# Kernel tuning notes

Measured on AMD Instinct MI355X. Metric: run time of the kernel, lower is better.

## Reference

```python
import jax, jax.numpy as jnp
import numpy as np

H, I, BS = 4096, 14336, 128   # hidden, intermediate, quant blocksize
B, S = 4, 2048                # batch, seq_len


def _dequant(w_int, s, blocksize):
    # w_int: [in, out] int8-valued weights; s: [in//blocksize, out] per-block scales.
    # Each contiguous block of `blocksize` input rows shares one scale.
    return w_int.astype(jnp.float32) * jnp.repeat(s, blocksize, axis=0)


def setup_inputs() -> dict:
    key = jax.random.key(0)
    k = jax.random.split(key, 7)
    x = jax.random.normal(k[0], (B, S, H), dtype=jnp.float32)
    w0 = jax.random.randint(k[1], (H, I), -127, 128, dtype=jnp.int32)  # gate proj (int8 values)
    w1 = jax.random.randint(k[2], (H, I), -127, 128, dtype=jnp.int32)  # up proj
    w2 = jax.random.randint(k[3], (I, H), -127, 128, dtype=jnp.int32)  # down proj
    # small positive per-block scales, typical magnitude for int8 weight quant
    s0 = jax.random.uniform(k[4], (H // BS, I), dtype=jnp.float32) * 0.02 + 1e-3
    s1 = jax.random.uniform(k[5], (H // BS, I), dtype=jnp.float32) * 0.02 + 1e-3
    s2 = jax.random.uniform(k[6], (I // BS, H), dtype=jnp.float32) * 0.02 + 1e-3
    return {"x": x, "w0": w0, "w1": w1, "w2": w2,
            "s0": s0, "s1": s1, "s2": s2, "blocksize": BS}


def reference(x, w0, w1, w2, s0, s1, s2, blocksize):
    # Fused w8a16 gated MLP: out = (silu(x @ W0) * (x @ W1)) @ W2
    W0 = _dequant(w0, s0, blocksize)  # [H, I]
    W1 = _dequant(w1, s1, blocksize)  # [H, I]
    W2 = _dequant(w2, s2, blocksize)  # [I, H]
    g = jnp.einsum('bsh,hi->bsi', x, W0)   # gate
    u = jnp.einsum('bsh,hi->bsi', x, W1)   # up
    h = jax.nn.silu(g) * u                 # [B, S, I]
    return jnp.einsum('bsi,ih->bsh', h, W2)  # same shape as x
```

## Files before the change

### kernel.cpp

```cpp
#include <hip/hip_runtime.h>
#include <cstdint>

#define H_DIM 4096
#define I_DIM 14336
#define M_TOT 8192
#define NI_DIM (2 * I_DIM)

typedef __bf16 bf16_t;
typedef bf16_t bf16x8_t __attribute__((ext_vector_type(8)));
typedef float f32x4_t __attribute__((ext_vector_type(4)));

#define AS1 __attribute__((address_space(1)))
#define AS3 __attribute__((address_space(3)))

static __device__ __forceinline__ unsigned short f2bf(float f) {
  union { float f; unsigned int u; } v; v.f = f;
  unsigned int r = ((v.u >> 16) & 1u) + 0x7FFFu;
  return (unsigned short)((v.u + r) >> 16);
}

static __device__ __forceinline__ void gl2lds16(const void* g, void* l) {
  __builtin_amdgcn_global_load_lds((AS1 void*)(void*)g, (AS3 void*)l, 16, 0, 0);
}

__global__ void k_cvt_x(const float* __restrict__ x,
                        unsigned short* __restrict__ xb, long n4) {
  long i = (long)blockIdx.x * blockDim.x + threadIdx.x;
  const long stride = (long)gridDim.x * blockDim.x;
  for (; i < n4; i += stride) {
    float4 v = ((const float4*)x)[i];
    ushort4 o;
    o.x = f2bf(v.x); o.y = f2bf(v.y); o.z = f2bf(v.z); o.w = f2bf(v.w);
    ((ushort4*)xb)[i] = o;
  }
}

__global__ void k_dequant_t(const int* __restrict__ w, const float* __restrict__ s,
                            unsigned short* __restrict__ wt, int K, int N,
                            int ioff) {
  __shared__ __align__(16) float tile[64 * 68];
  const int n0 = blockIdx.x * 64;
  const int k0 = blockIdx.y * 64;
  const int t = threadIdx.x;
  const int tx = t & 15;
  const int ty = t >> 4;
#pragma unroll
  for (int i = 0; i < 4; ++i) {
    const long gk = k0 + i * 16 + ty;
    const int4 wv = *(const int4*)(w + gk * N + (n0 + tx * 4));
    const float4 sv = *(const float4*)(s + (gk >> 7) * (long)N + (n0 + tx * 4));
    float4 o;
    o.x = (float)wv.x * sv.x;
    o.y = (float)wv.y * sv.y;
    o.z = (float)wv.z * sv.z;
    o.w = (float)wv.w * sv.w;
    *(float4*)(&tile[(i * 16 + ty) * 68 + tx * 4]) = o;
  }
  __syncthreads();
  const int nl = t >> 2;
  const int kc = (t & 3) << 4;
  unsigned int pk[8];
#pragma unroll
  for (int j = 0; j < 8; ++j) {
    unsigned int lo = f2bf(tile[(kc + 2 * j) * 68 + nl]);
    unsigned int hi = f2bf(tile[(kc + 2 * j + 1) * 68 + nl]);
    pk[j] = lo | (hi << 16);
  }
  const int n = n0 + nl;
  const long orow = (ioff < 0) ? (long)n
                               : (long)(((n >> 4) << 5) + (n & 15) + ioff);
  const long base = orow * K + (k0 + kc);
  uint4* dst = (uint4*)(wt + base);
  dst[0] = make_uint4(pk[0], pk[1], pk[2], pk[3]);
  dst[1] = make_uint4(pk[4], pk[5], pk[6], pk[7]);
}

template <int KDIM, int EPI>
__global__ __launch_bounds__(512, 1) void k_gemm_pipe(
    const unsigned short* __restrict__ A,
    const unsigned short* __restrict__ B,
    void* __restrict__ Cout, int Ntiles) {
  __shared__ __align__(16) unsigned short lds[3 * 24576];
  constexpr int KT = KDIM / 64;

  const int nwg = 32 * Ntiles;
  int id = blockIdx.x;
  id = (id & 7) * (nwg >> 3) + (id >> 3);
  const int per = 16 * Ntiles;
  const int grp = id / per;
  const int wi = id - grp * per;
  const int mt = grp * 16 + (wi & 15);
  const int nt = wi >> 4;
  const long m0 = (long)mt * 256;
  const long n0 = (long)nt * 128;

  const int t = threadIdx.x;
  const int lane = t & 63;
  const int wave = t >> 6;
  const int wm = wave >> 1;
  const int wn = wave & 1;

  const int srow = t >> 3;
  const int scol = (((t & 7) ^ (srow & 7)) << 3);
  const unsigned short* gA[4];
  const unsigned short* gB[2];
#pragma unroll
  for (int r = 0; r < 4; ++r)
    gA[r] = A + (m0 + r * 64 + srow) * (long)KDIM + scol;
#pragma unroll
  for (int r = 0; r < 2; ++r)
    gB[r] = B + (n0 + r * 64 + srow) * (long)KDIM + scol;
  unsigned short* sbase = &lds[wave * 512];

  const int colb = ((lane >> 4) ^ (lane & 7)) << 3;
  int aoff[4], boff[4];
#pragma unroll
  for (int mi = 0; mi < 4; ++mi)
    aoff[mi] = (wm * 64 + mi * 16 + (lane & 15)) * 64 + colb;
#pragma unroll
  for (int ni = 0; ni < 4; ++ni)
    boff[ni] = 16384 + (wn * 64 + ni * 16 + (lane & 15)) * 64 + colb;

  auto stage3A = [&](int kt2, int bs) {
    const long ko = (long)kt2 * 64;
    unsigned short* d = sbase + bs * 24576;
    gl2lds16(gA[0] + ko, d);
    gl2lds16(gA[1] + ko, d + 4096);
    gl2lds16(gA[2] + ko, d + 8192);
  };
  auto stage1A2B = [&](int kt2, int bs) {
    const long ko = (long)kt2 * 64;
    unsigned short* d = sbase + bs * 24576;
    gl2lds16(gA[3] + ko, d + 12288);
    gl2lds16(gB[0] + ko, d + 16384);
    gl2lds16(gB[1] + ko, d + 20480);
  };

  f32x4_t acc[4][4];
  const f32x4_t fz = {0.f, 0.f, 0.f, 0.f};
#pragma unroll
  for (int mi = 0; mi < 4; ++mi)
#pragma unroll
    for (int ni = 0; ni < 4; ++ni) acc[mi][ni] = fz;

  stage3A(0, 0); stage1A2B(0, 0);
  stage3A(1, 1); stage1A2B(1, 1);

  int bi = 0;
  for (int kt = 0; kt < KT; ++kt) {
    if (kt != KT - 1)
      asm volatile("s_waitcnt vmcnt(6)" ::: "memory");
    else
      asm volatile("s_waitcnt vmcnt(0)" ::: "memory");
    __builtin_amdgcn_s_barrier();

    const unsigned short* lb = &lds[bi * 24576];
    const int bs = (bi == 0) ? 2 : bi - 1;
    const bool pre = (kt + 2 < KT);

    bf16x8_t af[4], bfv[4];
#pragma unroll
    for (int mi = 0; mi < 4; ++mi) af[mi] = *(const bf16x8_t*)(lb + aoff[mi]);
#pragma unroll
    for (int ni = 0; ni < 4; ++ni) bfv[ni] = *(const bf16x8_t*)(lb + boff[ni]);
    if (pre) stage3A(kt + 2, bs);
    __builtin_amdgcn_s_barrier();
    asm volatile("s_waitcnt lgkmcnt(0)" ::: "memory");
    __builtin_amdgcn_sched_barrier(0);
    __builtin_amdgcn_s_setprio(1);
#pragma unroll
    for (int mi = 0; mi < 4; ++mi)
#pragma unroll
      for (int ni = 0; ni < 4; ++ni)
        acc[mi][ni] = __builtin_amdgcn_mfma_f32_16x16x32_bf16(
            af[mi], bfv[ni], acc[mi][ni], 0, 0, 0);
    __builtin_amdgcn_s_setprio(0);

#pragma unroll
    for (int mi = 0; mi < 4; ++mi)
      af[mi] = *(const bf16x8_t*)(lb + (aoff[mi] ^ 32));
#pragma unroll
    for (int ni = 0; ni < 4; ++ni)
      bfv[ni] = *(const bf16x8_t*)(lb + (boff[ni] ^ 32));
    if (pre) stage1A2B(kt + 2, bs);
    __builtin_amdgcn_s_barrier();
    asm volatile("s_waitcnt lgkmcnt(0)" ::: "memory");
    __builtin_amdgcn_sched_barrier(0);
    __builtin_amdgcn_s_setprio(1);
#pragma unroll
    for (int mi = 0; mi < 4; ++mi)
#pragma unroll
      for (int ni = 0; ni < 4; ++ni)
        acc[mi][ni] = __builtin_amdgcn_mfma_f32_16x16x32_bf16(
            af[mi], bfv[ni], acc[mi][ni], 0, 0, 0);
    __builtin_amdgcn_s_setprio(0);

    bi = (bi == 2) ? 0 : bi + 1;
  }

  const long mr0 = m0 + wm * 64 + ((lane >> 4) << 2);
  if constexpr (EPI == 1) {
    unsigned short* h = (unsigned short*)Cout;
    const int col0 = (int)(n0 >> 1) + wn * 32 + (lane & 15);
#pragma unroll
    for (int mi = 0; mi < 4; ++mi) {
#pragma unroll
      for (int p = 0; p < 2; ++p) {
        const long c = col0 + p * 16;
#pragma unroll
        for (int r = 0; r < 4; ++r) {
          const float gg = acc[mi][2 * p][r];
          const float uu = acc[mi][2 * p + 1][r];
          const float sg = gg / (1.0f + __expf(-gg));
          h[(mr0 + mi * 16 + r) * (long)I_DIM + c] = f2bf(sg * uu);
        }
      }
    }
  } else {
    float* o = (float*)Cout;
    const int col0 = (int)n0 + wn * 64 + (lane & 15);
#pragma unroll
    for (int mi = 0; mi < 4; ++mi)
#pragma unroll
      for (int ni = 0; ni < 4; ++ni)
#pragma unroll
        for (int r = 0; r < 4; ++r)
          o[(mr0 + mi * 16 + r) * (long)H_DIM + (col0 + ni * 16)] =
              acc[mi][ni][r];
  }
}

extern "C" void kernel_launch(void* const* d_in, const int* in_sizes, int n_in,
                              void* d_out, int out_size, void* d_ws, size_t ws_size,
                              hipStream_t stream) {
  const float* x  = (const float*)d_in[0];
  const int* w0   = (const int*)d_in[1];
  const int* w1   = (const int*)d_in[2];
  const int* w2   = (const int*)d_in[3];
  const float* s0 = (const float*)d_in[4];
  const float* s1 = (const float*)d_in[5];
  const float* s2 = (const float*)d_in[6];
  float* out = (float*)d_out;

  char* p = (char*)d_ws;
  unsigned short* xb   = (unsigned short*)p;
  unsigned short* w01t = (unsigned short*)(p + (long)M_TOT * H_DIM * 2);
  unsigned short* hb   = (unsigned short*)(p + (long)M_TOT * H_DIM * 2 +
                                           (long)NI_DIM * H_DIM * 2);
  unsigned short* w2t  = (unsigned short*)p;

  k_cvt_x<<<8192, 256, 0, stream>>>(x, xb, (long)M_TOT * H_DIM / 4);

  k_dequant_t<<<dim3(I_DIM / 64, H_DIM / 64), 256, 0, stream>>>(
      w0, s0, w01t, H_DIM, I_DIM, 0);
  k_dequant_t<<<dim3(I_DIM / 64, H_DIM / 64), 256, 0, stream>>>(
      w1, s1, w01t, H_DIM, I_DIM, 16);

  k_gemm_pipe<H_DIM, 1><<<(M_TOT / 256) * (NI_DIM / 128), 512, 0, stream>>>(
      xb, w01t, hb, NI_DIM / 128);

  k_dequant_t<<<dim3(H_DIM / 64, I_DIM / 64), 256, 0, stream>>>(
      w2, s2, w2t, I_DIM, H_DIM, -1);

  k_gemm_pipe<I_DIM, 2><<<(M_TOT / 256) * (H_DIM / 128), 512, 0, stream>>>(
      hb, w2t, out, H_DIM / 128);
}
```

Baseline: 3.436 ms.

## Switch GEMM to 256x256 tiles with 8-wave quadrant ping-pong pipeline

Replaces the 256x128 GEMM tile with a 256x256 tile where each of 8 waves computes a 128x64 sub-block (8x4 MFMA accumulators). The schedule becomes double-buffered LDS with four compute phases per k-step, each interleaving partial A/B reloads with global-to-LDS staging of the next tiles. The aim is to raise arithmetic intensity and cut global and LDS traffic per FLOP. The cost is more accumulator registers and 128KB of LDS, so effectively one workgroup per CU despite launch_bounds(512,2), plus more barriers per iteration.

```diff
diff --git a/kernel.cpp b/kernel.cpp
--- a/kernel.cpp
+++ b/kernel.cpp
@@ -76,11 +76,11 @@
 }
 
 template <int KDIM, int EPI>
-__global__ __launch_bounds__(512, 1) void k_gemm_pipe(
+__global__ __launch_bounds__(512, 2) void k_gemm8(
     const unsigned short* __restrict__ A,
     const unsigned short* __restrict__ B,
     void* __restrict__ Cout, int Ntiles) {
-  __shared__ __align__(16) unsigned short lds[3 * 24576];
+  __shared__ __align__(16) unsigned short lds[65536];
   constexpr int KT = KDIM / 64;
 
   const int nwg = 32 * Ntiles;
@@ -92,78 +92,76 @@
   const int mt = grp * 16 + (wi & 15);
   const int nt = wi >> 4;
   const long m0 = (long)mt * 256;
-  const long n0 = (long)nt * 128;
+  const long n0 = (long)nt * 256;
 
   const int t = threadIdx.x;
   const int lane = t & 63;
   const int wave = t >> 6;
-  const int wm = wave >> 1;
-  const int wn = wave & 1;
-
-  const int srow = t >> 3;
-  const int scol = (((t & 7) ^ (srow & 7)) << 3);
-  const unsigned short* gA[4];
-  const unsigned short* gB[2];
-#pragma unroll
-  for (int r = 0; r < 4; ++r)
-    gA[r] = A + (m0 + r * 64 + srow) * (long)KDIM + scol;
-#pragma unroll
-  for (int r = 0; r < 2; ++r)
-    gB[r] = B + (n0 + r * 64 + srow) * (long)KDIM + scol;
-  unsigned short* sbase = &lds[wave * 512];
-
-  const int colb = ((lane >> 4) ^ (lane & 7)) << 3;
-  int aoff[4], boff[4];
+  const int wm = wave >> 2;
+  const int wn = wave & 3;
+
+  const int srow = lane >> 3;
+  const int scol = ((lane & 7) ^ srow) << 3;
+  const unsigned short* pA = A + (m0 + wave * 16 + srow) * (long)KDIM + scol;
+  const unsigned short* pB = B + (n0 + wave * 16 + srow) * (long)KDIM + scol;
+  const int ldst = wave * 1024;
+
+  const int lr = lane & 15;
+  const int pch = ((lane >> 4) ^ (lane & 7)) << 3;
+  int aof[4], bof[4];
 #pragma unroll
   for (int mi = 0; mi < 4; ++mi)
-    aoff[mi] = (wm * 64 + mi * 16 + (lane & 15)) * 64 + colb;
-#pragma unroll
-  for (int ni = 0; ni < 4; ++ni)
-    boff[ni] = 16384 + (wn * 64 + ni * 16 + (lane & 15)) * 64 + colb;
-
-  auto stage3A = [&](int kt2, int bs) {
-    const long ko = (long)kt2 * 64;
-    unsigned short* d = sbase + bs * 24576;
-    gl2lds16(gA[0] + ko, d);
-    gl2lds16(gA[1] + ko, d + 4096);
-    gl2lds16(gA[2] + ko, d + 8192);
+    aof[mi] = wm * 8192 + (mi * 16 + lr) * 64 + pch;
+#pragma unroll
+  for (int nj = 0; nj < 4; ++nj)
+    bof[nj] = 16384 + (wn >> 1) * 8192 +
+              ((wn & 1) * 64 + nj * 16 + lr) * 64 + pch;
+
+  auto stgA = [&](int tile, int half, int buf) {
+    const long go = (long)half * 128 * KDIM + (long)tile * 64;
+    unsigned short* d = &lds[buf * 32768 + half * 8192 + ldst];
+    gl2lds16(pA + go, d);
+    gl2lds16(pA + go + 8 * (long)KDIM, d + 512);
   };
-  auto stage1A2B = [&](int kt2, int bs) {
-    const long ko = (long)kt2 * 64;
-    unsigned short* d = sbase + bs * 24576;
-    gl2lds16(gA[3] + ko, d + 12288);
-    gl2lds16(gB[0] + ko, d + 16384);
-    gl2lds16(gB[1] + ko, d + 20480);
+  auto stgB = [&](int tile, int half, int buf) {
+    const long go = (long)half * 128 * KDIM + (long)tile * 64;
+    unsigned short* d = &lds[buf * 32768 + 16384 + half * 8192 + ldst];
+    gl2lds16(pB + go, d);
+    gl2lds16(pB + go + 8 * (long)KDIM, d + 512);
   };
 
-  f32x4_t acc[4][4];
+  f32x4_t acc[8][4];
   const f32x4_t fz = {0.f, 0.f, 0.f, 0.f};
 #pragma unroll
-  for (int mi = 0; mi < 4; ++mi)
-#pragma unroll
-    for (int ni = 0; ni < 4; ++ni) acc[mi][ni] = fz;
-
-  stage3A(0, 0); stage1A2B(0, 0);
-  stage3A(1, 1); stage1A2B(1, 1);
-
-  int bi = 0;
+  for (int mi = 0; mi < 8; ++mi)
+#pragma unroll
+    for (int nj = 0; nj < 4; ++nj) acc[mi][nj] = fz;
+
+  stgB(0, 0, 0); stgB(0, 1, 0);
+  stgA(0, 0, 0); stgA(0, 1, 0);
+  stgB(1, 0, 1); stgB(1, 1, 1);
+  asm volatile("s_waitcnt vmcnt(4)" ::: "memory");
+  __builtin_amdgcn_s_barrier();
+
+  bf16x8_t af[4][2], b0[2][2], b1[2][2];
+
   for (int kt = 0; kt < KT; ++kt) {
-    if (kt != KT - 1)
-      asm volatile("s_waitcnt vmcnt(6)" ::: "memory");
-    else
-      asm volatile("s_waitcnt vmcnt(0)" ::: "memory");
-    __builtin_amdgcn_s_barrier();
-
-    const unsigned short* lb = &lds[bi * 24576];
-    const int bs = (bi == 0) ? 2 : bi - 1;
-    const bool pre = (kt + 2 < KT);
-
-    bf16x8_t af[4], bfv[4];
-#pragma unroll
-    for (int mi = 0; mi < 4; ++mi) af[mi] = *(const bf16x8_t*)(lb + aoff[mi]);
-#pragma unroll
-    for (int ni = 0; ni < 4; ++ni) bfv[ni] = *(const bf16x8_t*)(lb + boff[ni]);
-    if (pre) stage3A(kt + 2, bs);
+    const int cb = kt & 1;
+    const unsigned short* lb = &lds[cb * 32768];
+    const bool pa = (kt + 1 < KT);
+    const bool pb = (kt + 2 < KT);
+
+#pragma unroll
+    for (int mi = 0; mi < 4; ++mi) {
+      af[mi][0] = *(const bf16x8_t*)(lb + aof[mi]);
+      af[mi][1] = *(const bf16x8_t*)(lb + (aof[mi] ^ 32));
+    }
+#pragma unroll
+    for (int nj = 0; nj < 2; ++nj) {
+      b0[nj][0] = *(const bf16x8_t*)(lb + bof[nj]);
+      b0[nj][1] = *(const bf16x8_t*)(lb + (bof[nj] ^ 32));
+    }
+    if (pa) stgA(kt + 1, 0, cb ^ 1);
     __builtin_amdgcn_s_barrier();
     asm volatile("s_waitcnt lgkmcnt(0)" ::: "memory");
     __builtin_amdgcn_sched_barrier(0);
@@ -171,18 +169,20 @@
 #pragma unroll
     for (int mi = 0; mi < 4; ++mi)
 #pragma unroll
-      for (int ni = 0; ni < 4; ++ni)
-        acc[mi][ni] = __builtin_amdgcn_mfma_f32_16x16x32_bf16(
-            af[mi], bfv[ni], acc[mi][ni], 0, 0, 0);
+      for (int nj = 0; nj < 2; ++nj)
+#pragma unroll
+        for (int ks = 0; ks < 2; ++ks)
+          acc[mi][nj] = __builtin_amdgcn_mfma_f32_16x16x32_bf16(
+              af[mi][ks], b0[nj][ks], acc[mi][nj], 0, 0, 0);
     __builtin_amdgcn_s_setprio(0);
-
-#pragma unroll
-    for (int mi = 0; mi < 4; ++mi)
-      af[mi] = *(const bf16x8_t*)(lb + (aoff[mi] ^ 32));
-#pragma unroll
-    for (int ni = 0; ni < 4; ++ni)
-      bfv[ni] = *(const bf16x8_t*)(lb + (boff[ni] ^ 32));
-    if (pre) stage1A2B(kt + 2, bs);
+    __builtin_amdgcn_s_barrier();
+
+#pragma unroll
+    for (int nj = 0; nj < 2; ++nj) {
+      b1[nj][0] = *(const bf16x8_t*)(lb + bof[2 + nj]);
+      b1[nj][1] = *(const bf16x8_t*)(lb + (bof[2 + nj] ^ 32));
+    }
+    if (pa) stgA(kt + 1, 1, cb ^ 1);
     __builtin_amdgcn_s_barrier();
     asm volatile("s_waitcnt lgkmcnt(0)" ::: "memory");
     __builtin_amdgcn_sched_barrier(0);
@@ -190,27 +190,67 @@
 #pragma unroll
     for (int mi = 0; mi < 4; ++mi)
 #pragma unroll
-      for (int ni = 0; ni < 4; ++ni)
-        acc[mi][ni] = __builtin_amdgcn_mfma_f32_16x16x32_bf16(
-            af[mi], bfv[ni], acc[mi][ni], 0, 0, 0);
+      for (int nj = 0; nj < 2; ++nj)
+#pragma unroll
+        for (int ks = 0; ks < 2; ++ks)
+          acc[mi][2 + nj] = __builtin_amdgcn_mfma_f32_16x16x32_bf16(
+              af[mi][ks], b1[nj][ks], acc[mi][2 + nj], 0, 0, 0);
     __builtin_amdgcn_s_setprio(0);
-
-    bi = (bi == 2) ? 0 : bi + 1;
-  }
-
-  const long mr0 = m0 + wm * 64 + ((lane >> 4) << 2);
+    __builtin_amdgcn_s_barrier();
+
+#pragma unroll
+    for (int mi = 0; mi < 4; ++mi) {
+      af[mi][0] = *(const bf16x8_t*)(lb + (aof[mi] + 4096));
+      af[mi][1] = *(const bf16x8_t*)(lb + ((aof[mi] + 4096) ^ 32));
+    }
+    if (pb) stgB(kt + 2, 0, cb);
+    __builtin_amdgcn_s_barrier();
+    asm volatile("s_waitcnt lgkmcnt(0)" ::: "memory");
+    __builtin_amdgcn_sched_barrier(0);
+    __builtin_amdgcn_s_setprio(1);
+#pragma unroll
+    for (int mi = 0; mi < 4; ++mi)
+#pragma unroll
+      for (int nj = 0; nj < 2; ++nj)
+#pragma unroll
+        for (int ks = 0; ks < 2; ++ks)
+          acc[4 + mi][2 + nj] = __builtin_amdgcn_mfma_f32_16x16x32_bf16(
+              af[mi][ks], b1[nj][ks], acc[4 + mi][2 + nj], 0, 0, 0);
+    __builtin_amdgcn_s_setprio(0);
+    __builtin_amdgcn_s_barrier();
+
+    if (pb) stgB(kt + 2, 1, cb);
+    __builtin_amdgcn_s_barrier();
+    __builtin_amdgcn_s_setprio(1);
+#pragma unroll
+    for (int mi = 0; mi < 4; ++mi)
+#pragma unroll
+      for (int nj = 0; nj < 2; ++nj)
+#pragma unroll
+        for (int ks = 0; ks < 2; ++ks)
+          acc[4 + mi][nj] = __builtin_amdgcn_mfma_f32_16x16x32_bf16(
+              af[mi][ks], b0[nj][ks], acc[4 + mi][nj], 0, 0, 0);
+    __builtin_amdgcn_s_setprio(0);
+    if (pb)
+      asm volatile("s_waitcnt vmcnt(4)" ::: "memory");
+    else if (pa)
+      asm volatile("s_waitcnt vmcnt(0)" ::: "memory");
+    __builtin_amdgcn_s_barrier();
+  }
+
+  const long mr0 = m0 + wm * 128 + ((lane >> 4) << 2);
   if constexpr (EPI == 1) {
     unsigned short* h = (unsigned short*)Cout;
-    const int col0 = (int)(n0 >> 1) + wn * 32 + (lane & 15);
-#pragma unroll
-    for (int mi = 0; mi < 4; ++mi) {
-#pragma unroll
-      for (int p = 0; p < 2; ++p) {
-        const long c = col0 + p * 16;
+    const long col0 = (n0 >> 1) + wn * 32 + (lane & 15);
+#pragma unroll
+    for (int mi = 0; mi < 8; ++mi) {
+#pragma unroll
+      for (int k = 0; k < 2; ++k) {
+        const long c = col0 + k * 16;
 #pragma unroll
         for (int r = 0; r < 4; ++r) {
-          const float gg = acc[mi][2 * p][r];
-          const float uu = acc[mi][2 * p + 1][r];
+          const float gg = acc[mi][2 * k][r];
+          const float uu = acc[mi][2 * k + 1][r];
           const float sg = gg / (1.0f + __expf(-gg));
           h[(mr0 + mi * 16 + r) * (long)I_DIM + c] = f2bf(sg * uu);
         }
@@ -218,15 +258,15 @@
     }
   } else {
     float* o = (float*)Cout;
-    const int col0 = (int)n0 + wn * 64 + (lane & 15);
-#pragma unroll
-    for (int mi = 0; mi < 4; ++mi)
-#pragma unroll
-      for (int ni = 0; ni < 4; ++ni)
+    const long col0 = n0 + wn * 64 + (lane & 15);
+#pragma unroll
+    for (int mi = 0; mi < 8; ++mi)
+#pragma unroll
+      for (int nj = 0; nj < 4; ++nj)
 #pragma unroll
         for (int r = 0; r < 4; ++r)
-          o[(mr0 + mi * 16 + r) * (long)H_DIM + (col0 + ni * 16)] =
-              acc[mi][ni][r];
+          o[(mr0 + mi * 16 + r) * (long)H_DIM + (col0 + nj * 16)] =
+              acc[mi][nj][r];
   }
 }
 
@@ -256,12 +296,12 @@
   k_dequant_t<<<dim3(I_DIM / 64, H_DIM / 64), 256, 0, stream>>>(
       w1, s1, w01t, H_DIM, I_DIM, 16);
 
-  k_gemm_pipe<H_DIM, 1><<<(M_TOT / 256) * (NI_DIM / 128), 512, 0, stream>>>(
-      xb, w01t, hb, NI_DIM / 128);
+  k_gemm8<H_DIM, 1><<<(M_TOT / 256) * (NI_DIM / 256), 512, 0, stream>>>(
+      xb, w01t, hb, NI_DIM / 256);
 
   k_dequant_t<<<dim3(H_DIM / 64, I_DIM / 64), 256, 0, stream>>>(
       w2, s2, w2t, I_DIM, H_DIM, -1);
 
-  k_gemm_pipe<I_DIM, 2><<<(M_TOT / 256) * (H_DIM / 128), 512, 0, stream>>>(
-      hb, w2t, out, H_DIM / 128);
-}
+  k_gemm8<I_DIM, 2><<<(M_TOT / 256) * (H_DIM / 256), 512, 0, stream>>>(
+      hb, w2t, out, H_DIM / 256);
+}
```

Measured after the change: 2.992 ms. 12.9% less time.
